# Optimization experiments

Measured on AMD Instinct MI355X. Metric: run time of the kernel, lower is better.

Reference implementation:

```python
import jax, jax.numpy as jnp
import numpy as np

D, H, F, NL, B, TT, TS = 1024, 16, 4096, 4, 16, 128, 512
HD = D // H
NEG = -1e9


def layer_norm(x, s, b):
    m = x.mean(-1, keepdims=True)
    v = ((x - m) ** 2).mean(-1, keepdims=True)
    return (x - m) * jax.lax.rsqrt(v + 1e-5) * s + b


def setup_inputs() -> dict:
    key = jax.random.key(0)
    ks = jax.random.split(key, 28)
    text_encoded = jax.random.normal(ks[0], (TT, B, D), jnp.float32)
    speech_encoded = jax.random.normal(ks[1], (TS, B, D), jnp.float32)
    tlen = jax.random.randint(ks[2], (B,), 32, TT + 1)
    slen = jax.random.randint(ks[3], (B,), 128, TS + 1)
    text_padding_mask = jnp.arange(TT)[None, :] >= tlen[:, None]
    speech_padding_mask = jnp.arange(TS)[None, :] >= slen[:, None]
    sc = 0.02
    p = lambda k, sh: jax.random.normal(k, sh, jnp.float32) * sc
    return dict(
        text_encoded=text_encoded, speech_encoded=speech_encoded,
        text_padding_mask=text_padding_mask, speech_padding_mask=speech_padding_mask,
        cls_vector=p(ks[4], (D,)), sep_vector=p(ks[5], (D,)),
        Wq=p(ks[6], (NL, D, D)), bq=jnp.zeros((NL, D)),
        Wk=p(ks[7], (NL, D, D)), bk=jnp.zeros((NL, D)),
        Wv=p(ks[8], (NL, D, D)), bv=jnp.zeros((NL, D)),
        Wo=p(ks[9], (NL, D, D)), bo=jnp.zeros((NL, D)),
        ln1_s=jnp.ones((NL, D)), ln1_b=jnp.zeros((NL, D)),
        fc1_w=p(ks[10], (NL, D, F)), fc1_b=jnp.zeros((NL, F)),
        fc2_w=p(ks[11], (NL, F, D)), fc2_b=jnp.zeros((NL, D)),
        ln2_s=jnp.ones((NL, D)), ln2_b=jnp.zeros((NL, D)),
        out_w=p(ks[12], (1, D)),
    )


def _forward(text_encoded, speech_encoded, text_padding_mask, speech_padding_mask,
             cls_vector, sep_vector, Wq, bq, Wk, bk, Wv, bv, Wo, bo,
             ln1_s, ln1_b, fc1_w, fc1_b, fc2_w, fc2_b, ln2_s, ln2_b, out_w):
    Tt, Bb, d = text_encoded.shape
    Ts = speech_encoded.shape[0]
    L = Tt + Ts + 2  # static max concat length
    tlen = (~text_padding_mask).sum(-1)[:, None]   # [B,1]
    slen = (~speech_padding_mask).sum(-1)[:, None]  # [B,1]
    pos = jnp.arange(L)[None, :]                    # [1,L]
    is_cls = pos == 0
    is_text = (pos >= 1) & (pos < 1 + tlen)
    is_sep = pos == 1 + tlen
    is_speech = (pos >= 2 + tlen) & (pos < 2 + tlen + slen)
    # fused gather into the padded [B, L, D] buffer (replaces per-batch cat loop)
    text_bf = jnp.swapaxes(text_encoded, 0, 1)      # [B,Tt,D]
    speech_bf = jnp.swapaxes(speech_encoded, 0, 1)  # [B,Ts,D]
    t_idx = jnp.clip(pos - 1, 0, Tt - 1)
    s_idx = jnp.clip(pos - 2 - tlen, 0, Ts - 1)
    g_t = jnp.take_along_axis(text_bf, jnp.broadcast_to(t_idx[..., None], (Bb, L, 1)), axis=1)
    g_s = jnp.take_along_axis(speech_bf, jnp.broadcast_to(s_idx[..., None], (Bb, L, 1)), axis=1)
    x = jnp.where(is_cls[..., None], cls_vector,
        jnp.where(is_text[..., None], g_t,
        jnp.where(is_sep[..., None], sep_vector,
        jnp.where(is_speech[..., None], g_s, jnp.zeros((), x1 := text_encoded.dtype)))))  # [B,L,D]
    pad_mask = pos >= (2 + tlen + slen)             # [B,L] True = pad

    scale = HD ** -0.5
    for l in range(NL):  # post-norm fairseq encoder layers
        q = (x @ Wq[l] + bq[l]).reshape(Bb, L, H, HD) * scale
        k = (x @ Wk[l] + bk[l]).reshape(Bb, L, H, HD)
        v = (x @ Wv[l] + bv[l]).reshape(Bb, L, H, HD)
        scores = jnp.einsum('bqhd,bkhd->bhqk', q, k)
        scores = jnp.where(pad_mask[:, None, None, :], NEG, scores)
        attn = jax.nn.softmax(scores, axis=-1)
        o = jnp.einsum('bhqk,bkhd->bqhd', attn, v).reshape(Bb, L, D)
        x = layer_norm(x + (o @ Wo[l] + bo[l]), ln1_s[l], ln1_b[l])
        h = jax.nn.relu(x @ fc1_w[l] + fc1_b[l])
        x = layer_norm(x + (h @ fc2_w[l] + fc2_b[l]), ln2_s[l], ln2_b[l])
    return x[:, 0, :] @ out_w.T  # [B,1]


def reference(text_encoded, speech_encoded, text_padding_mask, speech_padding_mask,
              cls_vector, sep_vector, Wq, bq, Wk, bk, Wv, bv, Wo, bo,
              ln1_s, ln1_b, fc1_w, fc1_b, fc2_w, fc2_b, ln2_s, ln2_b, out_w):
    return _forward(text_encoded, speech_encoded, text_padding_mask, speech_padding_mask,
                    cls_vector, sep_vector, Wq, bq, Wk, bk, Wv, bv, Wo, bo,
                    ln1_s, ln1_b, fc1_w, fc1_b, fc2_w, fc2_b, ln2_s, ln2_b, out_w)
```

## Files before the change

kernel.cpp:

```cpp
#include <hip/hip_runtime.h>
#include <hip/hip_bf16.h>
#include <stdint.h>

#define D_   1024
#define H_   16
#define HD_  64
#define F_   4096
#define NL_  4
#define B_   16
#define TT_  128
#define TS_  512
#define LP_  704
#define M_   (B_*LP_)

typedef __attribute__((ext_vector_type(8)))  __bf16 bf16x8;
typedef __attribute__((ext_vector_type(4)))  float  floatx4;

typedef __attribute__((address_space(3))) void lds_void_t;
typedef const __attribute__((address_space(1))) void g_void_t;

__device__ __forceinline__ void gl2lds16(const __bf16* g, const __bf16* l) {
  __builtin_amdgcn_global_load_lds((g_void_t*)g, (lds_void_t*)l, 16, 0, 0);
}

__global__ void lens_kernel(const int* __restrict__ tmask, const int* __restrict__ smask,
                            int* __restrict__ lens) {
  __shared__ int red[256];
  int b = blockIdx.x, t = threadIdx.x;
  int tc = 0, sc = 0;
  if (t < TT_) tc = (tmask[b*TT_ + t] == 0) ? 1 : 0;
  for (int i = t; i < TS_; i += 256) sc += (smask[b*TS_ + i] == 0) ? 1 : 0;
  red[t] = tc + (sc << 16);
  __syncthreads();
  for (int s = 128; s > 0; s >>= 1) {
    if (t < s) red[t] += red[t + s];
    __syncthreads();
  }
  if (t == 0) {
    int tl = red[0] & 0xffff, sl = red[0] >> 16;
    if (tl < 0) tl = 0; if (tl > TT_) tl = TT_;
    if (sl < 0) sl = 0; if (sl > TS_) sl = TS_;
    int Lb = 2 + tl + sl;
    if (Lb > LP_) Lb = LP_;
    lens[2*b] = tl; lens[2*b+1] = Lb;
  }
}

__global__ void plan_kernel(const int* __restrict__ lens, int* __restrict__ plan) {
  if (threadIdx.x == 0 && blockIdx.x == 0) {
    int off = 0;
    for (int b = 0; b < B_; b++) {
      plan[2 + b] = off;
      int Lb = lens[2*b+1];
      int pad = ((Lb + 127) >> 7) << 7;
      if (pad > LP_) pad = LP_;
      off += pad;
    }
    plan[2 + B_] = off;
    plan[1] = off;
    plan[0] = (off + 127) >> 7;
  }
}

__global__ void transpose_kernel(const float* __restrict__ in, __bf16* __restrict__ out,
                                 int R, int C, long ozs) {
  __shared__ float tile[32][33];
  int x = threadIdx.x & 31, y0 = threadIdx.x >> 5;
  const float* inb = in + (size_t)blockIdx.z * R * C;
  __bf16* outb = out + (size_t)blockIdx.z * ozs;
  int r0 = blockIdx.y * 32, c0 = blockIdx.x * 32;
  #pragma unroll
  for (int i = 0; i < 4; i++) {
    int y = y0 + 8*i;
    tile[y][x] = inb[(size_t)(r0 + y)*C + c0 + x];
  }
  __syncthreads();
  #pragma unroll
  for (int i = 0; i < 4; i++) {
    int y = y0 + 8*i;
    outb[(size_t)(c0 + y)*R + r0 + x] = (__bf16)tile[x][y];
  }
}

__global__ void build_x_kernel(const float* __restrict__ text, const float* __restrict__ speech,
                               const float* __restrict__ cls, const float* __restrict__ sep,
                               const int* __restrict__ lens, const int* __restrict__ plan,
                               __bf16* __restrict__ xbf) {
  int b = blockIdx.y, l = blockIdx.x;
  int off = plan[2+b], padLb = plan[3+b] - off;
  if (l >= padLb) return;
  int tl = lens[2*b], Lb = lens[2*b+1];
  const float* src = nullptr;
  if (l == 0)              src = cls;
  else if (l <= tl)        src = text   + ((size_t)(l-1)*B_ + b)*D_;
  else if (l == tl + 1)    src = sep;
  else if (l < Lb)         src = speech + ((size_t)(l-2-tl)*B_ + b)*D_;
  __bf16* dst = xbf + (size_t)(off + l) * D_;
  #pragma unroll
  for (int j = 0; j < 4; j++) {
    int i = threadIdx.x + j*256;
    float v = src ? src[i] : 0.f;
    dst[i] = (__bf16)v;
  }
}

template<int MODE>
__global__ __launch_bounds__(256, 2)
void gemm_kernel(const __bf16* __restrict__ A, const __bf16* __restrict__ BT,
                 const float* __restrict__ bias, const float* __restrict__ bias2,
                 const float* __restrict__ bias3, void* __restrict__ Cv,
                 const int* __restrict__ plan, int Nn, int Kk, int Kloop, float scale) {
  if ((int)blockIdx.y >= plan[0]) return;
  __shared__ __bf16 As[128*32];
  __shared__ __bf16 Bs[128*32];
  int tid = threadIdx.x;
  int w = tid >> 6, l = tid & 63;
  int wm = w >> 1, wn = w & 1;
  long tile_m = (long)blockIdx.y * 128;
  long tile_n = (long)blockIdx.x * 128;
  long koff = (MODE == 6) ? (long)blockIdx.z * Kloop : 0;

  floatx4 acc[4][4] = {};

  const __bf16* ga = A  + (tile_m + w*32 + (l>>2)) * (long)Kk + (l&3)*8 + koff;
  const __bf16* gb = BT + (tile_n + w*32 + (l>>2)) * (long)Kk + (l&3)*8 + koff;
  const __bf16* lA = As + (w*32)*32;
  const __bf16* lB = Bs + (w*32)*32;

  int kcol = (l >> 4) * 8;
  const __bf16* afp = As + (wm*64 + (l&15))*32 + kcol;
  const __bf16* bfp = Bs + (wn*64 + (l&15))*32 + kcol;

  for (int k0 = 0; k0 < Kloop; k0 += 32) {
    gl2lds16(ga,               lA);
    gl2lds16(ga + 16*(long)Kk, lA + 16*32);
    gl2lds16(gb,               lB);
    gl2lds16(gb + 16*(long)Kk, lB + 16*32);
    ga += 32; gb += 32;
    __syncthreads();
    bf16x8 af[4], bf[4];
    #pragma unroll
    for (int mi = 0; mi < 4; mi++) af[mi] = *(const bf16x8*)(afp + mi*16*32);
    #pragma unroll
    for (int ni = 0; ni < 4; ni++) bf[ni] = *(const bf16x8*)(bfp + ni*16*32);
    #pragma unroll
    for (int mi = 0; mi < 4; mi++)
      #pragma unroll
      for (int ni = 0; ni < 4; ni++)
        acc[mi][ni] = __builtin_amdgcn_mfma_f32_16x16x32_bf16(af[mi], bf[ni], acc[mi][ni], 0, 0, 0);
    __syncthreads();
  }

  int rbase = wm*64 + (l>>4)*4;
  int cbase = wn*64 + (l&15);
  int seg = (int)(tile_n >> 10);
  float* outf = (float*)Cv;
  if (MODE == 6) outf += (long)blockIdx.z * ((long)M_ * D_);
  #pragma unroll
  for (int mi = 0; mi < 4; mi++) {
    long row0 = tile_m + rbase + mi*16;
    long voff = 0;
    int bb = 0;
    if (MODE == 5) {
      #pragma unroll
      for (int t = 1; t < B_; t++) bb += (row0 >= plan[2+t]) ? 1 : 0;
      voff = plan[2+bb];
    }
    #pragma unroll
    for (int ni = 0; ni < 4; ni++) {
      long col = tile_n + cbase + ni*16;
      float bv;
      if (MODE == 5) {
        const float* bp = (seg == 0) ? bias : (seg == 1) ? bias2 : bias3;
        bv = bp[col & 1023];
      } else if (MODE == 6) {
        bv = (blockIdx.z == 0) ? bias[col] : 0.f;
      } else {
        bv = bias[col];
      }
      #pragma unroll
      for (int r = 0; r < 4; r++) {
        long row = row0 + r;
        float v = acc[mi][ni][r] + bv;
        if (MODE == 2) v = v > 0.f ? v : 0.f;
        if (MODE == 0)      outf[row*Nn + col] = v;
        else if (MODE == 6) outf[row*Nn + col] = v;
        else if (MODE == 5) {
          __bf16* base = (__bf16*)Cv;
          long c = col & 1023;
          if (seg == 0)       base[row*D_ + c] = (__bf16)(v * scale);
          else if (seg == 1)  base[(long)M_*D_ + row*D_ + c] = (__bf16)v;
          else {
            long ll = row - voff;
            if (ll < LP_)
              base[2L*M_*D_ + (((long)bb*H_ + (c>>6))*HD_ + (c&63))*LP_ + ll] = (__bf16)v;
          }
        }
        else                ((__bf16*)Cv)[row*Nn + col] = (__bf16)v;
      }
    }
  }
}

__global__ __launch_bounds__(256, 2)
void attn_kernel(const __bf16* __restrict__ qb, const __bf16* __restrict__ kb,
                 const __bf16* __restrict__ vt, __bf16* __restrict__ ob,
                 const int* __restrict__ lens, const int* __restrict__ plan) {
  int col = blockIdx.x;
  int b = col >> 4;
  int off = plan[2+b];
  int padLb = plan[3+b] - off;
  if ((int)blockIdx.y * 128 >= padLb) return;
  __shared__ __bf16 Ks[64*64];
  __shared__ __bf16 Vs[64*64];
  __shared__ __bf16 Ps[4][32*72];
  int tid = threadIdx.x, w = tid >> 6, l = tid & 63;
  int Lb = lens[2*b+1];
  int q0w = blockIdx.y*128 + w*32;
  const size_t bh  = (size_t)off*D_ + (size_t)(col & 15)*HD_;
  const size_t vtb = (size_t)col * HD_ * LP_;
  int nkt = (Lb + 63) >> 6;

  bf16x8 qf[2][2];
  #pragma unroll
  for (int mi = 0; mi < 2; mi++) {
    int qr = q0w + mi*16 + (l&15);
    if (qr > padLb-1) qr = padLb-1;
    const __bf16* qp = qb + bh + (size_t)qr*D_ + (l>>4)*8;
    qf[mi][0] = *(const bf16x8*)(qp);
    qf[mi][1] = *(const bf16x8*)(qp + 32);
  }
  bf16x8 ones;
  #pragma unroll
  for (int j = 0; j < 8; j++) ones[j] = (__bf16)1.0f;

  floatx4 oacc[2][4] = {};
  floatx4 lacc[2] = {};

  for (int kt = 0; kt < nkt; kt++) {
    int kbase = kt*64;
    {
      int krow = w*16 + (l>>3);
      int cb = (l&7) ^ (krow & 7);
      const __bf16* gk = kb + bh + (size_t)(kbase + krow)*D_ + cb*8;
      const __bf16* lk = Ks + (w*16)*64;
      gl2lds16(gk,                lk);
      gl2lds16(gk + 8*(size_t)D_, lk + 8*64);
    }
    {
      int vrow = w*8 + (l>>3);
      int sb = (l&7) ^ (l>>3);
      const __bf16* gv = vt + vtb + (size_t)vrow*LP_ + kbase + sb*8;
      const __bf16* lv = Vs + (w*8)*64;
      gl2lds16(gv,                  lv);
      gl2lds16(gv + 32*(size_t)LP_, lv + 32*64);
    }
    __syncthreads();

    floatx4 s4[2][4] = {};
    #pragma unroll
    for (int ks = 0; ks < 2; ks++) {
      #pragma unroll
      for (int ni = 0; ni < 4; ni++) {
        int n = ni*16 + (l&15);
        int blk = (ks*4 + (l>>4)) ^ (n & 7);
        bf16x8 kf = *(const bf16x8*)(Ks + n*64 + blk*8);
        s4[0][ni] = __builtin_amdgcn_mfma_f32_16x16x32_bf16(qf[0][ks], kf, s4[0][ni], 0, 0, 0);
        s4[1][ni] = __builtin_amdgcn_mfma_f32_16x16x32_bf16(qf[1][ks], kf, s4[1][ni], 0, 0, 0);
      }
    }
    #pragma unroll
    for (int mi = 0; mi < 2; mi++) {
      #pragma unroll
      for (int ni = 0; ni < 4; ni++) {
        int key = kbase + ni*16 + (l&15);
        bool valid = key < Lb;
        #pragma unroll
        for (int r = 0; r < 4; r++) {
          float sv = valid ? fminf(s4[mi][ni][r], 30.f) : -1e9f;
          float p = __expf(sv);
          Ps[w][(mi*16 + (l>>4)*4 + r)*72 + ni*16 + (l&15)] = (__bf16)p;
        }
      }
    }
    #pragma unroll
    for (int ks = 0; ks < 2; ks++) {
      bf16x8 pf0 = *(const bf16x8*)(&Ps[w][(l&15)*72 + ks*32 + (l>>4)*8]);
      bf16x8 pf1 = *(const bf16x8*)(&Ps[w][(16 + (l&15))*72 + ks*32 + (l>>4)*8]);
      lacc[0] = __builtin_amdgcn_mfma_f32_16x16x32_bf16(pf0, ones, lacc[0], 0, 0, 0);
      lacc[1] = __builtin_amdgcn_mfma_f32_16x16x32_bf16(pf1, ones, lacc[1], 0, 0, 0);
      #pragma unroll
      for (int ni = 0; ni < 4; ni++) {
        int n = ni*16 + (l&15);
        int blk = (ks*4 + (l>>4)) ^ (n & 7);
        bf16x8 vf = *(const bf16x8*)(Vs + n*64 + blk*8);
        oacc[0][ni] = __builtin_amdgcn_mfma_f32_16x16x32_bf16(pf0, vf, oacc[0][ni], 0, 0, 0);
        oacc[1][ni] = __builtin_amdgcn_mfma_f32_16x16x32_bf16(pf1, vf, oacc[1][ni], 0, 0, 0);
      }
    }
    __syncthreads();
  }

  #pragma unroll
  for (int mi = 0; mi < 2; mi++) {
    #pragma unroll
    for (int ni = 0; ni < 4; ni++) {
      #pragma unroll
      for (int r = 0; r < 4; r++) {
        int qrow = q0w + mi*16 + (l>>4)*4 + r;
        if (qrow < padLb) {
          float ov = oacc[mi][ni][r] / lacc[mi][r];
          ob[bh + (size_t)qrow*D_ + ni*16 + (l&15)] = (__bf16)ov;
        }
      }
    }
  }
}

__global__ void ln_kernel(__bf16* __restrict__ x, const float* __restrict__ t,
                          const float* __restrict__ t2,
                          const float* __restrict__ sc, const float* __restrict__ bi,
                          const int* __restrict__ plan) {
  int row = blockIdx.x;
  if (row >= plan[1]) return;
  __shared__ float red[2][4];
  int tid = threadIdx.x;
  const float* tr = t + (size_t)row * D_;
  const float* tr2 = t2 ? t2 + (size_t)row * D_ : nullptr;
  __bf16* xr = x + (size_t)row * D_;
  float v[4], s1 = 0.f, s2 = 0.f;
  #pragma unroll
  for (int j = 0; j < 4; j++) {
    int i = tid + j*256;
    float val = (float)xr[i] + tr[i];
    if (tr2) val += tr2[i];
    v[j] = val; s1 += val; s2 += val*val;
  }
  #pragma unroll
  for (int off = 1; off < 64; off <<= 1) {
    s1 += __shfl_xor(s1, off, 64);
    s2 += __shfl_xor(s2, off, 64);
  }
  int w = tid >> 6, l = tid & 63;
  if (l == 0) { red[0][w] = s1; red[1][w] = s2; }
  __syncthreads();
  s1 = red[0][0] + red[0][1] + red[0][2] + red[0][3];
  s2 = red[1][0] + red[1][1] + red[1][2] + red[1][3];
  float mean = s1 * (1.f/D_);
  float var  = s2 * (1.f/D_) - mean*mean;
  float rstd = rsqrtf(var + 1e-5f);
  #pragma unroll
  for (int j = 0; j < 4; j++) {
    int i = tid + j*256;
    xr[i] = (__bf16)((v[j] - mean)*rstd*sc[i] + bi[i]);
  }
}

__global__ void out_kernel(const __bf16* __restrict__ x, const float* __restrict__ wv,
                           const int* __restrict__ plan, float* __restrict__ out) {
  __shared__ float red[4];
  int b = blockIdx.x, tid = threadIdx.x;
  const __bf16* xr = x + (size_t)plan[2+b] * D_;
  float s = 0.f;
  #pragma unroll
  for (int j = 0; j < 4; j++) {
    int i = tid + j*256;
    s += (float)xr[i] * wv[i];
  }
  #pragma unroll
  for (int off = 1; off < 64; off <<= 1) s += __shfl_xor(s, off, 64);
  int w = tid >> 6, l = tid & 63;
  if (l == 0) red[w] = s;
  __syncthreads();
  if (tid == 0) out[b] = red[0] + red[1] + red[2] + red[3];
}

extern "C" void kernel_launch(void* const* d_in, const int* in_sizes, int n_in,
                              void* d_out, int out_size, void* d_ws, size_t ws_size,
                              hipStream_t stream) {
  (void)in_sizes; (void)n_in; (void)out_size;
  const float* text   = (const float*)d_in[0];
  const float* speech = (const float*)d_in[1];
  const int*   tmask  = (const int*)d_in[2];
  const int*   smask  = (const int*)d_in[3];
  const float* cls    = (const float*)d_in[4];
  const float* sep    = (const float*)d_in[5];
  const float* Wq     = (const float*)d_in[6];
  const float* bq     = (const float*)d_in[7];
  const float* Wk     = (const float*)d_in[8];
  const float* bk     = (const float*)d_in[9];
  const float* Wv     = (const float*)d_in[10];
  const float* bv     = (const float*)d_in[11];
  const float* Wo     = (const float*)d_in[12];
  const float* bo     = (const float*)d_in[13];
  const float* ln1s   = (const float*)d_in[14];
  const float* ln1b   = (const float*)d_in[15];
  const float* fc1w   = (const float*)d_in[16];
  const float* fc1b   = (const float*)d_in[17];
  const float* fc2w   = (const float*)d_in[18];
  const float* fc2b   = (const float*)d_in[19];
  const float* ln2s   = (const float*)d_in[20];
  const float* ln2b   = (const float*)d_in[21];
  const float* outw   = (const float*)d_in[22];

  const size_t MD = (size_t)M_ * D_;
  char* ws = (char*)d_ws;
  int*    lens = (int*)ws;
  int*    plan = (int*)(ws + 128);
  __bf16* xbf  = (__bf16*)(ws + 256);
  __bf16* act  = (__bf16*)(ws + 256 + MD*2);
  float*  tmp  = (float*) (ws + 256 + MD*2 + 4*MD*2);
  __bf16* wt   = (__bf16*)(ws + 256 + MD*2 + 4*MD*2 + MD*4);

  __bf16* qb   = act;
  __bf16* kb   = act + MD;
  __bf16* vtG  = act + 2*MD;
  __bf16* obuf = act + 3*MD;
  __bf16* hb   = act;

  const size_t DD = (size_t)D_*D_;
  const size_t DF = (size_t)D_*F_;
  __bf16* wqkvT = wt;
  __bf16* woT   = wt + 12*DD;
  __bf16* fc1T  = wt + 16*DD;
  __bf16* fc2T  = wt + 16*DD + 4*DF;
  size_t wt_bytes = (16*DD + 8*DF) * sizeof(__bf16);
  float* tmp2 = (float*)((char*)wt + wt_bytes);
  size_t need2 = (256 + MD*2 + 4*MD*2 + MD*4) + wt_bytes + MD*4;
  const bool splitk = ws_size >= need2;

  lens_kernel<<<B_, 256, 0, stream>>>(tmask, smask, lens);
  plan_kernel<<<1, 64, 0, stream>>>(lens, plan);

  transpose_kernel<<<dim3(D_/32, D_/32, NL_), 256, 0, stream>>>(Wq, wqkvT,        D_, D_, 3*DD);
  transpose_kernel<<<dim3(D_/32, D_/32, NL_), 256, 0, stream>>>(Wk, wqkvT + DD,   D_, D_, 3*DD);
  transpose_kernel<<<dim3(D_/32, D_/32, NL_), 256, 0, stream>>>(Wv, wqkvT + 2*DD, D_, D_, 3*DD);
  transpose_kernel<<<dim3(D_/32, D_/32, NL_), 256, 0, stream>>>(Wo, woT,  D_, D_, DD);
  transpose_kernel<<<dim3(F_/32, D_/32, NL_), 256, 0, stream>>>(fc1w, fc1T, D_, F_, DF);
  transpose_kernel<<<dim3(D_/32, F_/32, NL_), 256, 0, stream>>>(fc2w, fc2T, F_, D_, DF);

  build_x_kernel<<<dim3(LP_, B_), 256, 0, stream>>>(text, speech, cls, sep, lens, plan, xbf);

  for (int lyr = 0; lyr < NL_; lyr++) {
    gemm_kernel<5><<<dim3(24, M_/128), 256, 0, stream>>>(
        xbf, wqkvT + (size_t)lyr*3*DD, bq + lyr*D_, bk + lyr*D_, bv + lyr*D_,
        act, plan, 3072, D_, D_, 0.125f);
    attn_kernel<<<dim3(B_*H_, (LP_+127)/128), 256, 0, stream>>>(qb, kb, vtG, obuf, lens, plan);
    gemm_kernel<0><<<dim3(D_/128, M_/128), 256, 0, stream>>>(
        obuf, woT + (size_t)lyr*DD, bo + lyr*D_, nullptr, nullptr, tmp, plan, D_, D_, D_, 1.f);
    ln_kernel<<<M_, 256, 0, stream>>>(xbf, tmp, nullptr, ln1s + lyr*D_, ln1b + lyr*D_, plan);
    gemm_kernel<2><<<dim3(F_/128, M_/128), 256, 0, stream>>>(
        xbf, fc1T + (size_t)lyr*DF, fc1b + lyr*F_, nullptr, nullptr, hb, plan, F_, D_, D_, 1.f);
    if (splitk) {
      gemm_kernel<6><<<dim3(D_/128, M_/128, 2), 256, 0, stream>>>(
          hb, fc2T + (size_t)lyr*DF, fc2b + lyr*D_, nullptr, nullptr, tmp, plan, D_, F_, 2048, 1.f);
      ln_kernel<<<M_, 256, 0, stream>>>(xbf, tmp, tmp2, ln2s + lyr*D_, ln2b + lyr*D_, plan);
    } else {
      gemm_kernel<6><<<dim3(D_/128, M_/128, 1), 256, 0, stream>>>(
          hb, fc2T + (size_t)lyr*DF, fc2b + lyr*D_, nullptr, nullptr, tmp, plan, D_, F_, F_, 1.f);
      ln_kernel<<<M_, 256, 0, stream>>>(xbf, tmp, nullptr, ln2s + lyr*D_, ln2b + lyr*D_, plan);
    }
  }

  out_kernel<<<B_, 256, 0, stream>>>(xbf, outw, plan, (float*)d_out);
}
```

Measured before the change: 1.748 ms.

## Replace 128x128 GEMM with pipelined 256x256 double-buffered swizzled GEMM

Replaces the simple 128x128 tile GEMM, which used a single LDS buffer and synchronized twice per 32-wide K step, with a 512-thread 256x256 tile kernel. The new kernel uses 64-wide K chunks, double-buffered XOR-swizzled LDS and phased prefetch with explicit waitcnt, barrier and setprio scheduling. Split-K for the FC2 GEMM is dropped in favour of the larger tile, and a zero-padding kernel is added so padded rows up to a multiple of 256 hold valid data. The larger tiles raise data reuse and cut LDS bank conflicts, but they launch fewer blocks and waste more work on padded rows.

Result: no change. 1.756 ms (+0.4%).

```diff
diff --git a/kernel.cpp b/kernel.cpp
--- a/kernel.cpp
+++ b/kernel.cpp
@@ -104,88 +104,219 @@
   }
 }
 
+__global__ void zpad_kernel(__bf16* __restrict__ xbf, __bf16* __restrict__ obuf,
+                            const int* __restrict__ plan) {
+  int mused = plan[1];
+  int mpad = (mused + 255) & ~255;
+  int r = mused + blockIdx.x;
+  if (r >= mpad) return;
+  __bf16* dst = (blockIdx.y == 0 ? xbf : obuf) + (size_t)r * D_;
+  #pragma unroll
+  for (int j = 0; j < 4; j++) dst[threadIdx.x + j*256] = (__bf16)0.f;
+}
+
+__device__ __forceinline__ void tile_phases(
+    const __bf16* AC, const __bf16* BC,
+    const __bf16* gA, const __bf16* gB, int Kk,
+    const __bf16* abDst, long abK, bool gAb,
+    const __bf16* aaDst, long aaK,
+    const __bf16* bDst,  long bK,  bool gNxt, int vmode,
+    int aBase, int bBase, int swzk0, int swzk1, int ldst,
+    floatx4 (&acc)[8][4])
+{
+  bf16x8 a[4][2], b0[2][2], b1[2][2];
+  #pragma unroll
+  for (int j = 0; j < 4; ++j) {
+    a[j][0] = *(const bf16x8*)(AC + aBase + j*1024 + swzk0);
+    a[j][1] = *(const bf16x8*)(AC + aBase + j*1024 + swzk1);
+  }
+  #pragma unroll
+  for (int n = 0; n < 2; ++n) {
+    b0[n][0] = *(const bf16x8*)(BC + bBase + n*1024 + swzk0);
+    b0[n][1] = *(const bf16x8*)(BC + bBase + n*1024 + swzk1);
+  }
+  if (gAb) {
+    gl2lds16(gA + 64*(long)Kk  + abK, abDst + 64*64  + ldst);
+    gl2lds16(gA + 192*(long)Kk + abK, abDst + 192*64 + ldst);
+  }
+  __builtin_amdgcn_s_barrier();
+  asm volatile("s_waitcnt lgkmcnt(0)" ::: "memory");
+  __builtin_amdgcn_sched_barrier(0);
+  __builtin_amdgcn_s_setprio(1);
+  #pragma unroll
+  for (int j = 0; j < 4; ++j)
+    #pragma unroll
+    for (int n = 0; n < 2; ++n) {
+      acc[j][n] = __builtin_amdgcn_mfma_f32_16x16x32_bf16(a[j][0], b0[n][0], acc[j][n], 0, 0, 0);
+      acc[j][n] = __builtin_amdgcn_mfma_f32_16x16x32_bf16(a[j][1], b0[n][1], acc[j][n], 0, 0, 0);
+    }
+  __builtin_amdgcn_s_setprio(0);
+  __builtin_amdgcn_s_barrier();
+  #pragma unroll
+  for (int n = 0; n < 2; ++n) {
+    b1[n][0] = *(const bf16x8*)(BC + bBase + (2+n)*1024 + swzk0);
+    b1[n][1] = *(const bf16x8*)(BC + bBase + (2+n)*1024 + swzk1);
+  }
+  if (gNxt) {
+    gl2lds16(gA + aaK,                aaDst + ldst);
+    gl2lds16(gA + 128*(long)Kk + aaK, aaDst + 128*64 + ldst);
+  }
+  __builtin_amdgcn_s_barrier();
+  asm volatile("s_waitcnt lgkmcnt(0)" ::: "memory");
+  __builtin_amdgcn_sched_barrier(0);
+  __builtin_amdgcn_s_setprio(1);
+  #pragma unroll
+  for (int j = 0; j < 4; ++j)
+    #pragma unroll
+    for (int n = 0; n < 2; ++n) {
+      acc[j][2+n] = __builtin_amdgcn_mfma_f32_16x16x32_bf16(a[j][0], b1[n][0], acc[j][2+n], 0, 0, 0);
+      acc[j][2+n] = __builtin_amdgcn_mfma_f32_16x16x32_bf16(a[j][1], b1[n][1], acc[j][2+n], 0, 0, 0);
+    }
+  __builtin_amdgcn_s_setprio(0);
+  __builtin_amdgcn_s_barrier();
+  #pragma unroll
+  for (int j = 0; j < 4; ++j) {
+    a[j][0] = *(const bf16x8*)(AC + aBase + 4096 + j*1024 + swzk0);
+    a[j][1] = *(const bf16x8*)(AC + aBase + 4096 + j*1024 + swzk1);
+  }
+  if (gNxt) {
+    gl2lds16(gB + bK,                bDst + ldst);
+    gl2lds16(gB + 64*(long)Kk + bK,  bDst + 64*64 + ldst);
+  }
+  __builtin_amdgcn_s_barrier();
+  asm volatile("s_waitcnt lgkmcnt(0)" ::: "memory");
+  __builtin_amdgcn_sched_barrier(0);
+  __builtin_amdgcn_s_setprio(1);
+  #pragma unroll
+  for (int j = 0; j < 4; ++j)
+    #pragma unroll
+    for (int n = 0; n < 2; ++n) {
+      acc[4+j][2+n] = __builtin_amdgcn_mfma_f32_16x16x32_bf16(a[j][0], b1[n][0], acc[4+j][2+n], 0, 0, 0);
+      acc[4+j][2+n] = __builtin_amdgcn_mfma_f32_16x16x32_bf16(a[j][1], b1[n][1], acc[4+j][2+n], 0, 0, 0);
+    }
+  __builtin_amdgcn_s_setprio(0);
+  __builtin_amdgcn_s_barrier();
+  if (gNxt) {
+    gl2lds16(gB + 128*(long)Kk + bK, bDst + 128*64 + ldst);
+    gl2lds16(gB + 192*(long)Kk + bK, bDst + 192*64 + ldst);
+  }
+  if (vmode == 6)      asm volatile("s_waitcnt vmcnt(6)" ::: "memory");
+  else if (vmode == 0) asm volatile("s_waitcnt vmcnt(0)" ::: "memory");
+  __builtin_amdgcn_s_barrier();
+  __builtin_amdgcn_s_setprio(1);
+  #pragma unroll
+  for (int j = 0; j < 4; ++j)
+    #pragma unroll
+    for (int n = 0; n < 2; ++n) {
+      acc[4+j][n] = __builtin_amdgcn_mfma_f32_16x16x32_bf16(a[j][0], b0[n][0], acc[4+j][n], 0, 0, 0);
+      acc[4+j][n] = __builtin_amdgcn_mfma_f32_16x16x32_bf16(a[j][1], b0[n][1], acc[4+j][n], 0, 0, 0);
+    }
+  __builtin_amdgcn_s_setprio(0);
+  __builtin_amdgcn_s_barrier();
+}
+
 template<int MODE>
-__global__ __launch_bounds__(256, 2)
-void gemm_kernel(const __bf16* __restrict__ A, const __bf16* __restrict__ BT,
-                 const float* __restrict__ bias, const float* __restrict__ bias2,
-                 const float* __restrict__ bias3, void* __restrict__ Cv,
-                 const int* __restrict__ plan, int Nn, int Kk, int Kloop, float scale) {
-  if ((int)blockIdx.y >= plan[0]) return;
-  __shared__ __bf16 As[128*32];
-  __shared__ __bf16 Bs[128*32];
-  int tid = threadIdx.x;
-  int w = tid >> 6, l = tid & 63;
-  int wm = w >> 1, wn = w & 1;
-  long tile_m = (long)blockIdx.y * 128;
-  long tile_n = (long)blockIdx.x * 128;
-  long koff = (MODE == 6) ? (long)blockIdx.z * Kloop : 0;
-
-  floatx4 acc[4][4] = {};
-
-  const __bf16* ga = A  + (tile_m + w*32 + (l>>2)) * (long)Kk + (l&3)*8 + koff;
-  const __bf16* gb = BT + (tile_n + w*32 + (l>>2)) * (long)Kk + (l&3)*8 + koff;
-  const __bf16* lA = As + (w*32)*32;
-  const __bf16* lB = Bs + (w*32)*32;
-
-  int kcol = (l >> 4) * 8;
-  const __bf16* afp = As + (wm*64 + (l&15))*32 + kcol;
-  const __bf16* bfp = Bs + (wn*64 + (l&15))*32 + kcol;
-
-  for (int k0 = 0; k0 < Kloop; k0 += 32) {
-    gl2lds16(ga,               lA);
-    gl2lds16(ga + 16*(long)Kk, lA + 16*32);
-    gl2lds16(gb,               lB);
-    gl2lds16(gb + 16*(long)Kk, lB + 16*32);
-    ga += 32; gb += 32;
-    __syncthreads();
-    bf16x8 af[4], bf[4];
-    #pragma unroll
-    for (int mi = 0; mi < 4; mi++) af[mi] = *(const bf16x8*)(afp + mi*16*32);
-    #pragma unroll
-    for (int ni = 0; ni < 4; ni++) bf[ni] = *(const bf16x8*)(bfp + ni*16*32);
-    #pragma unroll
-    for (int mi = 0; mi < 4; mi++)
-      #pragma unroll
-      for (int ni = 0; ni < 4; ni++)
-        acc[mi][ni] = __builtin_amdgcn_mfma_f32_16x16x32_bf16(af[mi], bf[ni], acc[mi][ni], 0, 0, 0);
-    __syncthreads();
-  }
-
-  int rbase = wm*64 + (l>>4)*4;
-  int cbase = wn*64 + (l&15);
-  int seg = (int)(tile_n >> 10);
+__global__ __launch_bounds__(512, 2)
+void gemm256_kernel(const __bf16* __restrict__ A, const __bf16* __restrict__ BT,
+                    const float* __restrict__ bias, const float* __restrict__ bias2,
+                    const float* __restrict__ bias3, void* __restrict__ Cv,
+                    const int* __restrict__ plan, int Nn, int Kk, int Kloop, float scale) {
+  const int mused = plan[1];
+  if ((int)blockIdx.y * 256 >= mused) return;
+  __shared__ __align__(16) __bf16 smem[65536];
+  __bf16* lA0 = smem;
+  __bf16* lB0 = smem + 16384;
+  __bf16* lA1 = smem + 32768;
+  __bf16* lB1 = smem + 49152;
+  const int tid = threadIdx.x;
+  const int w = tid >> 6, l = tid & 63;
+  const int wm = w >> 2, wn = w & 3;
+  const long tile_m = (long)blockIdx.y * 256;
+  const long tile_n = (long)blockIdx.x * 256;
+
+  int pofs[16];
+  if (MODE == 5) {
+    #pragma unroll
+    for (int t = 0; t < 16; ++t) pofs[t] = plan[2 + t];
+  }
+
+  const int srow = tid >> 3;
+  const int scol = ((tid & 7) * 16) ^ ((srow & 7) << 4);
+  const __bf16* gA = A  + (tile_m + srow) * (long)Kk + (scol >> 1);
+  const __bf16* gB = BT + (tile_n + srow) * (long)Kk + (scol >> 1);
+  const int ldst = w * 512;
+
+  gl2lds16(gA,                     lA0 + ldst);
+  gl2lds16(gA + 128*(long)Kk,      lA0 + 128*64 + ldst);
+  gl2lds16(gB,                     lB0 + ldst);
+  gl2lds16(gB + 64*(long)Kk,       lB0 + 64*64  + ldst);
+  gl2lds16(gB + 128*(long)Kk,      lB0 + 128*64 + ldst);
+  gl2lds16(gB + 192*(long)Kk,      lB0 + 192*64 + ldst);
+  gl2lds16(gA + 64*(long)Kk,       lA0 + 64*64  + ldst);
+  gl2lds16(gA + 192*(long)Kk,      lA0 + 192*64 + ldst);
+  gl2lds16(gA + 64,                lA1 + ldst);
+  gl2lds16(gA + 128*(long)Kk + 64, lA1 + 128*64 + ldst);
+  gl2lds16(gB + 64,                lB1 + ldst);
+  gl2lds16(gB + 64*(long)Kk + 64,  lB1 + 64*64  + ldst);
+  gl2lds16(gB + 128*(long)Kk + 64, lB1 + 128*64 + ldst);
+  gl2lds16(gB + 192*(long)Kk + 64, lB1 + 192*64 + ldst);
+  asm volatile("s_waitcnt vmcnt(6)" ::: "memory");
+  __builtin_amdgcn_s_barrier();
+
+  const int aBase = (wm*128 + (l & 15)) * 64;
+  const int bBase = (wn*64  + (l & 15)) * 64;
+  const int swzk0 = (((l >> 4) * 16)      ^ ((l & 7) << 4)) >> 1;
+  const int swzk1 = ((64 + (l >> 4) * 16) ^ ((l & 7) << 4)) >> 1;
+
+  floatx4 acc[8][4] = {};
+
+  const int NIT = Kloop >> 7;
+  for (int it = 0; it < NIT; ++it) {
+    const bool more = (it + 1 < NIT);
+    const long kof = (long)it * 128;
+    tile_phases(lA0, lB0, gA, gB, Kk,
+                lA1, kof + 64, true,
+                lA0, kof + 128,
+                lB0, kof + 128, more, more ? 6 : 0,
+                aBase, bBase, swzk0, swzk1, ldst, acc);
+    tile_phases(lA1, lB1, gA, gB, Kk,
+                lA0, kof + 128, more,
+                lA1, kof + 192,
+                lB1, kof + 192, more, more ? 6 : -1,
+                aBase, bBase, swzk0, swzk1, ldst, acc);
+  }
+
+  const int rl4 = (l >> 4) * 4, cl = l & 15;
+  const int seg = (int)(tile_n >> 10);
   float* outf = (float*)Cv;
-  if (MODE == 6) outf += (long)blockIdx.z * ((long)M_ * D_);
-  #pragma unroll
-  for (int mi = 0; mi < 4; mi++) {
-    long row0 = tile_m + rbase + mi*16;
+  #pragma unroll
+  for (int mi = 0; mi < 8; ++mi) {
+    long row0 = tile_m + wm*128 + mi*16 + rl4;
     long voff = 0;
     int bb = 0;
     if (MODE == 5) {
       #pragma unroll
-      for (int t = 1; t < B_; t++) bb += (row0 >= plan[2+t]) ? 1 : 0;
-      voff = plan[2+bb];
-    }
-    #pragma unroll
-    for (int ni = 0; ni < 4; ni++) {
-      long col = tile_n + cbase + ni*16;
+      for (int t = 1; t < B_; t++) bb += (row0 >= pofs[t]) ? 1 : 0;
+      voff = pofs[bb];
+    }
+    #pragma unroll
+    for (int ni = 0; ni < 4; ++ni) {
+      long col = tile_n + wn*64 + ni*16 + cl;
       float bv;
       if (MODE == 5) {
         const float* bp = (seg == 0) ? bias : (seg == 1) ? bias2 : bias3;
         bv = bp[col & 1023];
-      } else if (MODE == 6) {
-        bv = (blockIdx.z == 0) ? bias[col] : 0.f;
       } else {
         bv = bias[col];
       }
       #pragma unroll
-      for (int r = 0; r < 4; r++) {
+      for (int r = 0; r < 4; ++r) {
         long row = row0 + r;
         float v = acc[mi][ni][r] + bv;
         if (MODE == 2) v = v > 0.f ? v : 0.f;
         if (MODE == 0)      outf[row*Nn + col] = v;
-        else if (MODE == 6) outf[row*Nn + col] = v;
-        else if (MODE == 5) {
+        else if (MODE == 2) ((__bf16*)Cv)[row*Nn + col] = (__bf16)v;
+        else {
           __bf16* base = (__bf16*)Cv;
           long c = col & 1023;
           if (seg == 0)       base[row*D_ + c] = (__bf16)(v * scale);
@@ -196,7 +327,6 @@
               base[2L*M_*D_ + (((long)bb*H_ + (c>>6))*HD_ + (c&63))*LP_ + ll] = (__bf16)v;
           }
         }
-        else                ((__bf16*)Cv)[row*Nn + col] = (__bf16)v;
       }
     }
   }
@@ -378,7 +508,7 @@
 extern "C" void kernel_launch(void* const* d_in, const int* in_sizes, int n_in,
                               void* d_out, int out_size, void* d_ws, size_t ws_size,
                               hipStream_t stream) {
-  (void)in_sizes; (void)n_in; (void)out_size;
+  (void)in_sizes; (void)n_in; (void)out_size; (void)ws_size;
   const float* text   = (const float*)d_in[0];
   const float* speech = (const float*)d_in[1];
   const int*   tmask  = (const int*)d_in[2];
@@ -424,10 +554,6 @@
   __bf16* woT   = wt + 12*DD;
   __bf16* fc1T  = wt + 16*DD;
   __bf16* fc2T  = wt + 16*DD + 4*DF;
-  size_t wt_bytes = (16*DD + 8*DF) * sizeof(__bf16);
-  float* tmp2 = (float*)((char*)wt + wt_bytes);
-  size_t need2 = (256 + MD*2 + 4*MD*2 + MD*4) + wt_bytes + MD*4;
-  const bool splitk = ws_size >= need2;
 
   lens_kernel<<<B_, 256, 0, stream>>>(tmask, smask, lens);
   plan_kernel<<<1, 64, 0, stream>>>(lens, plan);
@@ -440,26 +566,21 @@
   transpose_kernel<<<dim3(D_/32, F_/32, NL_), 256, 0, stream>>>(fc2w, fc2T, F_, D_, DF);
 
   build_x_kernel<<<dim3(LP_, B_), 256, 0, stream>>>(text, speech, cls, sep, lens, plan, xbf);
+  zpad_kernel<<<dim3(128, 2), 256, 0, stream>>>(xbf, obuf, plan);
 
   for (int lyr = 0; lyr < NL_; lyr++) {
-    gemm_kernel<5><<<dim3(24, M_/128), 256, 0, stream>>>(
+    gemm256_kernel<5><<<dim3(12, M_/256), 512, 0, stream>>>(
         xbf, wqkvT + (size_t)lyr*3*DD, bq + lyr*D_, bk + lyr*D_, bv + lyr*D_,
         act, plan, 3072, D_, D_, 0.125f);
     attn_kernel<<<dim3(B_*H_, (LP_+127)/128), 256, 0, stream>>>(qb, kb, vtG, obuf, lens, plan);
-    gemm_kernel<0><<<dim3(D_/128, M_/128), 256, 0, stream>>>(
+    gemm256_kernel<0><<<dim3(D_/256, M_/256), 512, 0, stream>>>(
         obuf, woT + (size_t)lyr*DD, bo + lyr*D_, nullptr, nullptr, tmp, plan, D_, D_, D_, 1.f);
     ln_kernel<<<M_, 256, 0, stream>>>(xbf, tmp, nullptr, ln1s + lyr*D_, ln1b + lyr*D_, plan);
-    gemm_kernel<2><<<dim3(F_/128, M_/128), 256, 0, stream>>>(
+    gemm256_kernel<2><<<dim3(F_/256, M_/256), 512, 0, stream>>>(
         xbf, fc1T + (size_t)lyr*DF, fc1b + lyr*F_, nullptr, nullptr, hb, plan, F_, D_, D_, 1.f);
-    if (splitk) {
-      gemm_kernel<6><<<dim3(D_/128, M_/128, 2), 256, 0, stream>>>(
-          hb, fc2T + (size_t)lyr*DF, fc2b + lyr*D_, nullptr, nullptr, tmp, plan, D_, F_, 2048, 1.f);
-      ln_kernel<<<M_, 256, 0, stream>>>(xbf, tmp, tmp2, ln2s + lyr*D_, ln2b + lyr*D_, plan);
-    } else {
-      gemm_kernel<6><<<dim3(D_/128, M_/128, 1), 256, 0, stream>>>(
-          hb, fc2T + (size_t)lyr*DF, fc2b + lyr*D_, nullptr, nullptr, tmp, plan, D_, F_, F_, 1.f);
-      ln_kernel<<<M_, 256, 0, stream>>>(xbf, tmp, nullptr, ln2s + lyr*D_, ln2b + lyr*D_, plan);
-    }
+    gemm256_kernel<0><<<dim3(D_/256, M_/256), 512, 0, stream>>>(
+        hb, fc2T + (size_t)lyr*DF, fc2b + lyr*D_, nullptr, nullptr, tmp, plan, D_, F_, F_, 1.f);
+    ln_kernel<<<M_, 256, 0, stream>>>(xbf, tmp, nullptr, ln2s + lyr*D_, ln2b + lyr*D_, plan);
   }
 
   out_kernel<<<B_, 256, 0, stream>>>(xbf, outw, plan, (float*)d_out);
```
